# Kernel tuning notes

Measured on AMD Instinct MI355X. Metric: run time of the kernel, lower is better.

The kernel has to match this reference:

```python
import jax, jax.numpy as jnp
import numpy as np


def setup_inputs() -> dict:
    key = jax.random.key(0)
    ks = jax.random.split(key, 6)
    B, T, S, E, D = 8, 128, 512, 512, 512  # batch, trg_len, src_len, enc_dim, trg_dim
    W_SCALE = 0.03  # small init to keep tanh unsaturated
    return {
        "hidden": jax.random.normal(ks[0], (B, T, D), jnp.float32),
        "encoder_outputs": jax.random.normal(ks[1], (B, S, E), jnp.float32),
        "encoder_mask": jnp.ones((B, S), jnp.float32),
        "W_attn": jax.random.normal(ks[2], (D, E + D), jnp.float32) * W_SCALE,
        "b_attn": jnp.zeros((D,), jnp.float32),
        "W_v": jax.random.normal(ks[3], (1, D), jnp.float32) * W_SCALE,
        "b_v": jnp.zeros((1,), jnp.float32),
        "W_out": jax.random.normal(ks[4], (D, E + D), jnp.float32) * W_SCALE,
    }


def masked_softmax(x, m, axis=-1):
    # faithful to repo: x*m, stable exp, e*m, normalize with eps
    x = x * m
    e_x = jnp.exp(x - jnp.max(x, axis=axis, keepdims=True))
    e_x = e_x * m
    return e_x / (jnp.sum(e_x, axis=axis, keepdims=True) + 1e-6)


def reference(hidden, encoder_outputs, encoder_mask, W_attn, b_attn, W_v, b_v, W_out):
    B, T, D = hidden.shape
    S = encoder_outputs.shape[1]
    # concat order in get_energy is (hidden_i, encoder_outputs), so split W_attn
    W_h = W_attn[:, :D]   # (D_out, trg_dim)
    W_e = W_attn[:, D:]   # (D_out, enc_dim)
    # Linear(concat) == h@W_h^T + e@W_e^T + b; vectorized over all (t, s) pairs
    hp = jnp.einsum('btd,kd->btk', hidden, W_h)            # (B,T,K)
    ep = jnp.einsum('bse,ke->bsk', encoder_outputs, W_e)   # (B,S,K)
    feat = jnp.tanh(hp[:, :, None, :] + ep[:, None, :, :] + b_attn)  # (B,T,S,K)
    energies = jnp.einsum('btsk,k->bts', feat, W_v[0]) + b_v[0]      # (B,T,S)
    # forward: energies * mask, then masked softmax
    m = encoder_mask[:, None, :]  # (B,1,S)
    energies = energies * m
    attn_weights = masked_softmax(energies, m, axis=-1)    # (B,T,S)
    weighted_context = jnp.einsum('bts,bse->bte', attn_weights, encoder_outputs)
    h_cat = jnp.concatenate([weighted_context, hidden], axis=-1)  # (B,T,E+D)
    h_tilde = jnp.tanh(jnp.einsum('btc,dc->btd', h_cat, W_out))   # (B,T,D)
    return h_tilde, weighted_context, attn_weights
```

## Files before the change

kernel.cpp:

```cpp
#include <hip/hip_runtime.h>
#include <hip/hip_bf16.h>
#include <math.h>

typedef unsigned short u16;
typedef unsigned int u32;
typedef __bf16 bf16x8 __attribute__((ext_vector_type(8)));
typedef float f32x4 __attribute__((ext_vector_type(4)));

#define OUT_WC   524288LL
#define OUT_ATTN 1048576LL
#define C2 2.8853900817779268f
#define LOG2E 1.4426950408889634f
#define LAS 40

__device__ inline u16 f2b(float f) {
    return (u16)((__float_as_uint(f) + 0x8000u) >> 16);
}
__device__ inline float b2f(u16 v) { return __uint_as_float(((u32)v) << 16); }
__device__ inline u32 pkcvt(float x, float y) {
    __hip_bfloat162 h = __float22bfloat162_rn(make_float2(x, y));
    return *(u32*)&h;
}
__device__ inline float tanh_fast(float x) {
    return 1.f - 2.f * __builtin_amdgcn_rcpf(__builtin_amdgcn_exp2f(C2 * x) + 1.f);
}

__global__ __launch_bounds__(256) void tobf(
    const float* __restrict__ enc, const float* __restrict__ hidden,
    const float* __restrict__ Wattn, const float* __restrict__ Wout,
    u16* __restrict__ dst)
{
    long long i = ((long long)blockIdx.x * 256 + threadIdx.x) * 8;
    const float* src; long long off;
    if (i < 2097152)      { src = enc;    off = i; }
    else if (i < 2621440) { src = hidden; off = i - 2097152; }
    else if (i < 3145728) { src = Wattn;  off = i - 2621440; }
    else                  { src = Wout;   off = i - 3145728; }
    float4 v0 = *(const float4*)(src + off);
    float4 v1 = *(const float4*)(src + off + 4);
    *(uint4*)(dst + i) = make_uint4(pkcvt(v0.x, v0.y), pkcvt(v0.z, v0.w),
                                    pkcvt(v1.x, v1.y), pkcvt(v1.z, v1.w));
}

__global__ __launch_bounds__(256) void proj(
    const u16* __restrict__ hidden_bf, const u16* __restrict__ enc_bf,
    const u16* __restrict__ Wattn_bf, const float* __restrict__ battn,
    const u16* __restrict__ Wout_bf,
    float* __restrict__ hp, u16* __restrict__ ept, float* __restrict__ hh)
{
    __shared__ u16 lA[64 * LAS];
    __shared__ u16 lB[64 * LAS];
    const int tid = threadIdx.x;
    const int wvi = tid >> 6, ln = tid & 63;
    const int wm = wvi >> 1, wn = wvi & 1;
    const int l16 = ln & 15, quad = ln >> 4;
    const int blk = blockIdx.x;
    int bx, by, zz = 0, lda, ldb, mode;
    const u16 *A, *B;
    if (blk < 512) {
        mode = 0;
        zz = blk >> 6; by = (blk >> 3) & 7; bx = blk & 7;
        A = Wattn_bf + 512; lda = 1024;
        B = enc_bf + (long long)zz * 262144; ldb = 512;
    } else if (blk < 640) {
        mode = 1;
        int i = blk - 512; by = i >> 3; bx = i & 7;
        A = hidden_bf; lda = 512;
        B = Wattn_bf; ldb = 1024;
    } else {
        mode = 2;
        int i = blk - 640; by = i >> 3; bx = i & 7;
        A = hidden_bf; lda = 512;
        B = Wout_bf + 512; ldb = 1024;
    }
    const int m0 = by * 64, n0 = bx * 64;
    const int srow = tid >> 2, skof = (tid & 3) * 8;
    const u16* Ap = A + (long long)(m0 + srow) * lda + skof;
    const u16* Bp = B + (long long)(n0 + srow) * ldb + skof;

    f32x4 acc00 = {0,0,0,0}, acc01 = {0,0,0,0}, acc10 = {0,0,0,0}, acc11 = {0,0,0,0};

    for (int k0 = 0; k0 < 512; k0 += 32) {
        uint4 av = *(const uint4*)(Ap + k0);
        uint4 bv = *(const uint4*)(Bp + k0);
        __syncthreads();
        *(uint4*)&lA[srow * LAS + skof] = av;
        *(uint4*)&lB[srow * LAS + skof] = bv;
        __syncthreads();
        bf16x8 a0 = *(const bf16x8*)&lA[(wm * 32      + l16) * LAS + quad * 8];
        bf16x8 a1 = *(const bf16x8*)&lA[(wm * 32 + 16 + l16) * LAS + quad * 8];
        bf16x8 b0 = *(const bf16x8*)&lB[(wn * 32      + l16) * LAS + quad * 8];
        bf16x8 b1 = *(const bf16x8*)&lB[(wn * 32 + 16 + l16) * LAS + quad * 8];
        acc00 = __builtin_amdgcn_mfma_f32_16x16x32_bf16(a0, b0, acc00, 0, 0, 0);
        acc01 = __builtin_amdgcn_mfma_f32_16x16x32_bf16(a0, b1, acc01, 0, 0, 0);
        acc10 = __builtin_amdgcn_mfma_f32_16x16x32_bf16(a1, b0, acc10, 0, 0, 0);
        acc11 = __builtin_amdgcn_mfma_f32_16x16x32_bf16(a1, b1, acc11, 0, 0, 0);
    }

    const f32x4* accs[4] = { &acc00, &acc01, &acc10, &acc11 };
    #pragma unroll
    for (int i = 0; i < 2; ++i) {
        #pragma unroll
        for (int j = 0; j < 2; ++j) {
            const f32x4& a = *accs[i * 2 + j];
            #pragma unroll
            for (int r = 0; r < 4; ++r) {
                int m = m0 + wm * 32 + i * 16 + quad * 4 + r;
                int n = n0 + wn * 32 + j * 16 + l16;
                float v = a[r];
                if (mode == 0)
                    ept[(long long)zz * 262144 + (long long)m * 512 + n] =
                        f2b(__builtin_amdgcn_exp2f(C2 * v));
                else if (mode == 1)
                    hp[(long long)m * 512 + n] = C2 * (v + battn[n]);
                else
                    hh[(long long)m * 512 + n] = v;
            }
        }
    }
}

__device__ inline float wred_sum(float v) {
    #pragma unroll
    for (int i = 32; i > 0; i >>= 1) v += __shfl_xor(v, i);
    return v;
}
__device__ inline float wred_max(float v) {
    #pragma unroll
    for (int i = 32; i > 0; i >>= 1) v = fmaxf(v, __shfl_xor(v, i));
    return v;
}

__device__ inline void proc8(uint4 c, float4 hw, float* a0, float* a1) {
    u32 cc[4] = {c.x, c.y, c.z, c.w};
    #pragma unroll
    for (int i = 0; i < 4; ++i) {
        float xl = __uint_as_float(cc[i] << 16);
        float xh = __uint_as_float(cc[i] & 0xFFFF0000u);
        float rl0 = __builtin_amdgcn_rcpf(fmaf(hw.x, xl, 1.f));
        float rh0 = __builtin_amdgcn_rcpf(fmaf(hw.x, xh, 1.f));
        float rl1 = __builtin_amdgcn_rcpf(fmaf(hw.y, xl, 1.f));
        float rh1 = __builtin_amdgcn_rcpf(fmaf(hw.y, xh, 1.f));
        a0[2*i]   = fmaf(hw.z, rl0, a0[2*i]);
        a0[2*i+1] = fmaf(hw.z, rh0, a0[2*i+1]);
        a1[2*i]   = fmaf(hw.z, rl1, a1[2*i]);
        a1[2*i+1] = fmaf(hw.z, rh1, a1[2*i+1]);
    }
}
__device__ inline void wcproc2(uint4 c, float2 ap, float* acc0, float* acc1) {
    u32 cc[4] = {c.x, c.y, c.z, c.w};
    #pragma unroll
    for (int i = 0; i < 4; ++i) {
        float el = __uint_as_float(cc[i] << 16);
        float eh = __uint_as_float(cc[i] & 0xFFFF0000u);
        acc0[2*i]   = fmaf(ap.x, el, acc0[2*i]);
        acc0[2*i+1] = fmaf(ap.x, eh, acc0[2*i+1]);
        acc1[2*i]   = fmaf(ap.y, el, acc1[2*i]);
        acc1[2*i+1] = fmaf(ap.y, eh, acc1[2*i+1]);
    }
}

__global__ __launch_bounds__(1024) void energies(
    const float* __restrict__ maskp, const float* __restrict__ hp,
    const u16* __restrict__ ept, const float* __restrict__ Wv,
    const float* __restrict__ bvp, const u16* __restrict__ enc_bf,
    float* __restrict__ attn, float* __restrict__ wc)
{
    __shared__ __align__(16) float4 hpw[512];
    __shared__ float pa[2][16][512];
    __shared__ float aL[512][2];
    __shared__ float red[16];
    const int tid = threadIdx.x;
    const int b  = blockIdx.x & 7;
    const int t0 = (blockIdx.x >> 3) * 2;
    const int th = tid >> 9;
    const int k5 = tid & 511;
    const long long row0 = (long long)(b * 128 + t0) * 512;

    float hv = hp[row0 + (long long)th * 512 + k5];
    float eh = __builtin_amdgcn_exp2f(hv);
    float* hpwf = (float*)hpw;
    hpwf[k5 * 4 + th] = eh;
    float w = 0.f;
    if (th == 0) { w = Wv[k5]; hpwf[k5 * 4 + 2] = w; }
    float wsum = wred_sum(w);
    if ((tid & 63) == 0) red[tid >> 6] = wsum;
    __syncthreads();
    float sumWv = 0.f;
    #pragma unroll
    for (int i = 0; i < 16; ++i) sumWv += red[i];

    const int kg = tid >> 6, sl = tid & 63;
    const int s0 = sl * 8;
    const u16* eb = ept + (long long)b * 262144 + (kg * 32) * 512 + s0;
    const float4* hq = &hpw[kg * 32];

    float a0[8] = {0,0,0,0,0,0,0,0}, a1[8] = {0,0,0,0,0,0,0,0};
    uint4 c0 = *(const uint4*)(eb);
    uint4 c1 = *(const uint4*)(eb + 512);
    for (int kk = 0; kk < 30; kk += 2) {
        const u16* nb = eb + (kk + 2) * 512;
        uint4 n0 = *(const uint4*)(nb);
        uint4 n1 = *(const uint4*)(nb + 512);
        proc8(c0, hq[kk],     a0, a1);
        proc8(c1, hq[kk + 1], a0, a1);
        c0 = n0; c1 = n1;
    }
    proc8(c0, hq[30], a0, a1);
    proc8(c1, hq[31], a0, a1);

    *(float4*)&pa[0][kg][s0]     = make_float4(a0[0], a0[1], a0[2], a0[3]);
    *(float4*)&pa[0][kg][s0 + 4] = make_float4(a0[4], a0[5], a0[6], a0[7]);
    *(float4*)&pa[1][kg][s0]     = make_float4(a1[0], a1[1], a1[2], a1[3]);
    *(float4*)&pa[1][kg][s0 + 4] = make_float4(a1[4], a1[5], a1[6], a1[7]);
    __syncthreads();

    float A = 0.f;
    #pragma unroll
    for (int g = 0; g < 16; ++g) A += pa[th][g][k5];
    float mv = maskp[(long long)b * 512 + k5];
    float bv0 = bvp[0];
    float r = (bv0 + sumWv - 2.f * A) * mv; r *= mv;

    float vmax = wred_max(r);
    if ((tid & 63) == 0) red[tid >> 6] = vmax;
    __syncthreads();
    float mx = red[th * 8];
    #pragma unroll
    for (int i = 1; i < 8; ++i) mx = fmaxf(mx, red[th * 8 + i]);

    float ex = __builtin_amdgcn_exp2f((r - mx) * LOG2E) * mv;
    float vsum = wred_sum(ex);
    __syncthreads();
    if ((tid & 63) == 0) red[tid >> 6] = vsum;
    __syncthreads();
    float sm = 0.f;
    #pragma unroll
    for (int i = 0; i < 8; ++i) sm += red[th * 8 + i];
    float at = ex * (1.f / (sm + 1e-6f));
    attn[row0 + (long long)th * 512 + k5] = at;
    aL[k5][th] = at;
    __syncthreads();

    const int eg = tid & 63, sg = tid >> 6;
    const u16* encb = enc_bf + (long long)b * 262144 + (long long)(sg * 32) * 512 + eg * 8;
    const float2* aq = (const float2*)&aL[sg * 32][0];
    float acc0[8] = {0,0,0,0,0,0,0,0}, acc1[8] = {0,0,0,0,0,0,0,0};
    uint4 e0 = *(const uint4*)(encb);
    uint4 e1 = *(const uint4*)(encb + 512);
    for (int j = 0; j < 30; j += 2) {
        uint4 f0 = *(const uint4*)(encb + (long long)(j + 2) * 512);
        uint4 f1 = *(const uint4*)(encb + (long long)(j + 3) * 512);
        wcproc2(e0, aq[j],     acc0, acc1);
        wcproc2(e1, aq[j + 1], acc0, acc1);
        e0 = f0; e1 = f1;
    }
    wcproc2(e0, aq[30], acc0, acc1);
    wcproc2(e1, aq[31], acc0, acc1);

    *(float4*)&pa[0][sg][eg * 8]     = make_float4(acc0[0], acc0[1], acc0[2], acc0[3]);
    *(float4*)&pa[0][sg][eg * 8 + 4] = make_float4(acc0[4], acc0[5], acc0[6], acc0[7]);
    *(float4*)&pa[1][sg][eg * 8]     = make_float4(acc1[0], acc1[1], acc1[2], acc1[3]);
    *(float4*)&pa[1][sg][eg * 8 + 4] = make_float4(acc1[4], acc1[5], acc1[6], acc1[7]);
    __syncthreads();

    float wcv = 0.f;
    #pragma unroll
    for (int g = 0; g < 16; ++g) wcv += pa[th][g][k5];
    wc[row0 + (long long)th * 512 + k5] = wcv;
}

__global__ __launch_bounds__(256) void hout_k(
    const float* __restrict__ wc, const u16* __restrict__ Wout_bf,
    float* __restrict__ out)
{
    __shared__ u16 lA[32 * LAS];
    __shared__ u16 lB[64 * LAS];
    const int tid = threadIdx.x;
    const int wvi = tid >> 6, ln = tid & 63;
    const int l16 = ln & 15, quad = ln >> 4;
    const int msub = wvi & 1, npair = wvi >> 1;
    const int m0 = blockIdx.y * 32, n0 = blockIdx.x * 64;
    const int rowA = tid >> 3, kofA = (tid & 7) * 4;
    const int rowB = tid >> 2, kofB = (tid & 3) * 8;
    f32x4 acc0 = {0,0,0,0}, acc1 = {0,0,0,0};

    for (int k0 = 0; k0 < 512; k0 += 32) {
        float4 av = *(const float4*)(wc + (long long)(m0 + rowA) * 512 + k0 + kofA);
        uint4 bv = *(const uint4*)(Wout_bf + (long long)(n0 + rowB) * 1024 + k0 + kofB);
        __syncthreads();
        *(uint2*)&lA[rowA * LAS + kofA] = make_uint2(pkcvt(av.x, av.y), pkcvt(av.z, av.w));
        int kk = kofB ^ (((rowB >> 3) & 3) << 3);
        *(uint4*)&lB[rowB * LAS + kk] = bv;
        __syncthreads();
        bf16x8 a = *(const bf16x8*)&lA[(msub * 16 + l16) * LAS + quad * 8];
        int nr0 = npair * 32 + l16, nr1 = nr0 + 16;
        bf16x8 b0 = *(const bf16x8*)&lB[nr0 * LAS + (quad * 8 ^ (((nr0 >> 3) & 3) << 3))];
        bf16x8 b1 = *(const bf16x8*)&lB[nr1 * LAS + (quad * 8 ^ (((nr1 >> 3) & 3) << 3))];
        acc0 = __builtin_amdgcn_mfma_f32_16x16x32_bf16(a, b0, acc0, 0, 0, 0);
        acc1 = __builtin_amdgcn_mfma_f32_16x16x32_bf16(a, b1, acc1, 0, 0, 0);
    }
    #pragma unroll
    for (int j = 0; j < 2; ++j) {
        const f32x4& a = j ? acc1 : acc0;
        #pragma unroll
        for (int r = 0; r < 4; ++r) {
            int m = m0 + msub * 16 + quad * 4 + r;
            int n = n0 + npair * 32 + j * 16 + l16;
            long long idx = (long long)m * 512 + n;
            out[idx] = tanh_fast(a[r] + out[idx]);
        }
    }
}

extern "C" void kernel_launch(void* const* d_in, const int* in_sizes, int n_in,
                              void* d_out, int out_size, void* d_ws, size_t ws_size,
                              hipStream_t stream)
{
    const float* hidden = (const float*)d_in[0];
    const float* enc    = (const float*)d_in[1];
    const float* mask   = (const float*)d_in[2];
    const float* Wattn  = (const float*)d_in[3];
    const float* battn  = (const float*)d_in[4];
    const float* Wv     = (const float*)d_in[5];
    const float* bvp    = (const float*)d_in[6];
    const float* Wout   = (const float*)d_in[7];
    float* out = (float*)d_out;

    float* hp  = (float*)d_ws;
    u16*   ept = (u16*)((char*)d_ws + (2 << 20));
    u16*   bfp = (u16*)((char*)d_ws + (6 << 20));
    u16* enc_bf    = bfp;
    u16* hidden_bf = bfp + 2097152;
    u16* Wattn_bf  = bfp + 2621440;
    u16* Wout_bf   = bfp + 3145728;

    tobf<<<1792, 256, 0, stream>>>(enc, hidden, Wattn, Wout, bfp);
    proj<<<768, 256, 0, stream>>>(hidden_bf, enc_bf, Wattn_bf, battn, Wout_bf,
                                  hp, ept, out );
    energies<<<512, 1024, 0, stream>>>(mask, hp, ept, Wv, bvp, enc_bf,
                                       out + OUT_ATTN, out + OUT_WC);
    hout_k<<<dim3(8, 32, 1), 256, 0, stream>>>(out + OUT_WC, Wout_bf, out);
}
```

Before: 146.6 us.

## Fuse bf16 conversion into GEMM loads and use LDS atomics for reductions

Removes the separate fp32-to-bf16 conversion kernel. The projection and output GEMMs now load fp32 directly and convert in registers, and one set of projection blocks writes the bf16 copy of encoder outputs for later use. In the energies kernel, the large 16-way partial-sum LDS buffer is replaced by a small accumulator updated with shared-memory atomicAdd. This cuts LDS footprint, which may raise occupancy, at the cost of atomic contention and doubled global read bytes in the GEMMs.

Measured after the change: 226.5 us. 54.5% more time.

```diff
diff --git a/kernel.cpp b/kernel.cpp
--- a/kernel.cpp
+++ b/kernel.cpp
@@ -25,28 +25,12 @@
     return 1.f - 2.f * __builtin_amdgcn_rcpf(__builtin_amdgcn_exp2f(C2 * x) + 1.f);
 }
 
-__global__ __launch_bounds__(256) void tobf(
-    const float* __restrict__ enc, const float* __restrict__ hidden,
-    const float* __restrict__ Wattn, const float* __restrict__ Wout,
-    u16* __restrict__ dst)
-{
-    long long i = ((long long)blockIdx.x * 256 + threadIdx.x) * 8;
-    const float* src; long long off;
-    if (i < 2097152)      { src = enc;    off = i; }
-    else if (i < 2621440) { src = hidden; off = i - 2097152; }
-    else if (i < 3145728) { src = Wattn;  off = i - 2621440; }
-    else                  { src = Wout;   off = i - 3145728; }
-    float4 v0 = *(const float4*)(src + off);
-    float4 v1 = *(const float4*)(src + off + 4);
-    *(uint4*)(dst + i) = make_uint4(pkcvt(v0.x, v0.y), pkcvt(v0.z, v0.w),
-                                    pkcvt(v1.x, v1.y), pkcvt(v1.z, v1.w));
-}
-
 __global__ __launch_bounds__(256) void proj(
-    const u16* __restrict__ hidden_bf, const u16* __restrict__ enc_bf,
-    const u16* __restrict__ Wattn_bf, const float* __restrict__ battn,
-    const u16* __restrict__ Wout_bf,
-    float* __restrict__ hp, u16* __restrict__ ept, float* __restrict__ hh)
+    const float* __restrict__ hidden, const float* __restrict__ enc,
+    const float* __restrict__ Wattn, const float* __restrict__ battn,
+    const float* __restrict__ Wout,
+    float* __restrict__ hp, u16* __restrict__ ept, float* __restrict__ hh,
+    u16* __restrict__ enc_bf)
 {
     __shared__ u16 lA[64 * LAS];
     __shared__ u16 lB[64 * LAS];
@@ -56,33 +40,43 @@
     const int l16 = ln & 15, quad = ln >> 4;
     const int blk = blockIdx.x;
     int bx, by, zz = 0, lda, ldb, mode;
-    const u16 *A, *B;
+    const float *A, *B;
     if (blk < 512) {
         mode = 0;
         zz = blk >> 6; by = (blk >> 3) & 7; bx = blk & 7;
-        A = Wattn_bf + 512; lda = 1024;
-        B = enc_bf + (long long)zz * 262144; ldb = 512;
+        A = Wattn + 512; lda = 1024;
+        B = enc + (long long)zz * 262144; ldb = 512;
     } else if (blk < 640) {
         mode = 1;
         int i = blk - 512; by = i >> 3; bx = i & 7;
-        A = hidden_bf; lda = 512;
-        B = Wattn_bf; ldb = 1024;
+        A = hidden; lda = 512;
+        B = Wattn; ldb = 1024;
     } else {
         mode = 2;
         int i = blk - 640; by = i >> 3; bx = i & 7;
-        A = hidden_bf; lda = 512;
-        B = Wout_bf + 512; ldb = 1024;
+        A = hidden; lda = 512;
+        B = Wout + 512; ldb = 1024;
     }
     const int m0 = by * 64, n0 = bx * 64;
     const int srow = tid >> 2, skof = (tid & 3) * 8;
-    const u16* Ap = A + (long long)(m0 + srow) * lda + skof;
-    const u16* Bp = B + (long long)(n0 + srow) * ldb + skof;
+    const float* Ap = A + (long long)(m0 + srow) * lda + skof;
+    const float* Bp = B + (long long)(n0 + srow) * ldb + skof;
+    const bool wr_enc = (mode == 0) && (by == 0);
 
     f32x4 acc00 = {0,0,0,0}, acc01 = {0,0,0,0}, acc10 = {0,0,0,0}, acc11 = {0,0,0,0};
 
     for (int k0 = 0; k0 < 512; k0 += 32) {
-        uint4 av = *(const uint4*)(Ap + k0);
-        uint4 bv = *(const uint4*)(Bp + k0);
+        float4 af0 = *(const float4*)(Ap + k0);
+        float4 af1 = *(const float4*)(Ap + k0 + 4);
+        float4 bf0 = *(const float4*)(Bp + k0);
+        float4 bf1 = *(const float4*)(Bp + k0 + 4);
+        uint4 av = make_uint4(pkcvt(af0.x, af0.y), pkcvt(af0.z, af0.w),
+                              pkcvt(af1.x, af1.y), pkcvt(af1.z, af1.w));
+        uint4 bv = make_uint4(pkcvt(bf0.x, bf0.y), pkcvt(bf0.z, bf0.w),
+                              pkcvt(bf1.x, bf1.y), pkcvt(bf1.z, bf1.w));
+        if (wr_enc)
+            *(uint4*)(enc_bf + (long long)zz * 262144 +
+                      (long long)(n0 + srow) * 512 + k0 + skof) = bv;
         __syncthreads();
         *(uint4*)&lA[srow * LAS + skof] = av;
         *(uint4*)&lB[srow * LAS + skof] = bv;
@@ -167,7 +161,7 @@
     float* __restrict__ attn, float* __restrict__ wc)
 {
     __shared__ __align__(16) float4 hpw[512];
-    __shared__ float pa[2][16][512];
+    __shared__ float accE[2][512];
     __shared__ float aL[512][2];
     __shared__ float red[16];
     const int tid = threadIdx.x;
@@ -177,10 +171,11 @@
     const int k5 = tid & 511;
     const long long row0 = (long long)(b * 128 + t0) * 512;
 
+    ((float*)accE)[tid] = 0.f;
     float hv = hp[row0 + (long long)th * 512 + k5];
-    float eh = __builtin_amdgcn_exp2f(hv);
+    float ehv = __builtin_amdgcn_exp2f(hv);
     float* hpwf = (float*)hpw;
-    hpwf[k5 * 4 + th] = eh;
+    hpwf[k5 * 4 + th] = ehv;
     float w = 0.f;
     if (th == 0) { w = Wv[k5]; hpwf[k5 * 4 + 2] = w; }
     float wsum = wred_sum(w);
@@ -209,15 +204,15 @@
     proc8(c0, hq[30], a0, a1);
     proc8(c1, hq[31], a0, a1);
 
-    *(float4*)&pa[0][kg][s0]     = make_float4(a0[0], a0[1], a0[2], a0[3]);
-    *(float4*)&pa[0][kg][s0 + 4] = make_float4(a0[4], a0[5], a0[6], a0[7]);
-    *(float4*)&pa[1][kg][s0]     = make_float4(a1[0], a1[1], a1[2], a1[3]);
-    *(float4*)&pa[1][kg][s0 + 4] = make_float4(a1[4], a1[5], a1[6], a1[7]);
-    __syncthreads();
-
-    float A = 0.f;
-    #pragma unroll
-    for (int g = 0; g < 16; ++g) A += pa[th][g][k5];
+    #pragma unroll
+    for (int i = 0; i < 8; ++i) {
+        int ii = (i + sl) & 7;
+        atomicAdd(&accE[0][s0 + ii], a0[ii]);
+        atomicAdd(&accE[1][s0 + ii], a1[ii]);
+    }
+    __syncthreads();
+
+    float A = accE[th][k5];
     float mv = maskp[(long long)b * 512 + k5];
     float bv0 = bvp[0];
     float r = (bv0 + sumWv - 2.f * A) * mv; r *= mv;
@@ -240,6 +235,7 @@
     float at = ex * (1.f / (sm + 1e-6f));
     attn[row0 + (long long)th * 512 + k5] = at;
     aL[k5][th] = at;
+    ((float*)accE)[tid] = 0.f;
     __syncthreads();
 
     const int eg = tid & 63, sg = tid >> 6;
@@ -258,20 +254,19 @@
     wcproc2(e0, aq[30], acc0, acc1);
     wcproc2(e1, aq[31], acc0, acc1);
 
-    *(float4*)&pa[0][sg][eg * 8]     = make_float4(acc0[0], acc0[1], acc0[2], acc0[3]);
-    *(float4*)&pa[0][sg][eg * 8 + 4] = make_float4(acc0[4], acc0[5], acc0[6], acc0[7]);
-    *(float4*)&pa[1][sg][eg * 8]     = make_float4(acc1[0], acc1[1], acc1[2], acc1[3]);
-    *(float4*)&pa[1][sg][eg * 8 + 4] = make_float4(acc1[4], acc1[5], acc1[6], acc1[7]);
-    __syncthreads();
-
-    float wcv = 0.f;
-    #pragma unroll
-    for (int g = 0; g < 16; ++g) wcv += pa[th][g][k5];
-    wc[row0 + (long long)th * 512 + k5] = wcv;
+    #pragma unroll
+    for (int i = 0; i < 8; ++i) {
+        int ii = (i + eg) & 7;
+        atomicAdd(&accE[0][eg * 8 + ii], acc0[ii]);
+        atomicAdd(&accE[1][eg * 8 + ii], acc1[ii]);
+    }
+    __syncthreads();
+
+    wc[row0 + (long long)th * 512 + k5] = accE[th][k5];
 }
 
 __global__ __launch_bounds__(256) void hout_k(
-    const float* __restrict__ wc, const u16* __restrict__ Wout_bf,
+    const float* __restrict__ wc, const float* __restrict__ Wout,
     float* __restrict__ out)
 {
     __shared__ u16 lA[32 * LAS];
@@ -287,7 +282,10 @@
 
     for (int k0 = 0; k0 < 512; k0 += 32) {
         float4 av = *(const float4*)(wc + (long long)(m0 + rowA) * 512 + k0 + kofA);
-        uint4 bv = *(const uint4*)(Wout_bf + (long long)(n0 + rowB) * 1024 + k0 + kofB);
+        float4 bw0 = *(const float4*)(Wout + (long long)(n0 + rowB) * 1024 + k0 + kofB);
+        float4 bw1 = *(const float4*)(Wout + (long long)(n0 + rowB) * 1024 + k0 + kofB + 4);
+        uint4 bv = make_uint4(pkcvt(bw0.x, bw0.y), pkcvt(bw0.z, bw0.w),
+                              pkcvt(bw1.x, bw1.y), pkcvt(bw1.z, bw1.w));
         __syncthreads();
         *(uint2*)&lA[rowA * LAS + kofA] = make_uint2(pkcvt(av.x, av.y), pkcvt(av.z, av.w));
         int kk = kofB ^ (((rowB >> 3) & 3) << 3);
@@ -327,18 +325,13 @@
     const float* Wout   = (const float*)d_in[7];
     float* out = (float*)d_out;
 
-    float* hp  = (float*)d_ws;
-    u16*   ept = (u16*)((char*)d_ws + (2 << 20));
-    u16*   bfp = (u16*)((char*)d_ws + (6 << 20));
-    u16* enc_bf    = bfp;
-    u16* hidden_bf = bfp + 2097152;
-    u16* Wattn_bf  = bfp + 2621440;
-    u16* Wout_bf   = bfp + 3145728;
-
-    tobf<<<1792, 256, 0, stream>>>(enc, hidden, Wattn, Wout, bfp);
-    proj<<<768, 256, 0, stream>>>(hidden_bf, enc_bf, Wattn_bf, battn, Wout_bf,
-                                  hp, ept, out );
+    float* hp     = (float*)d_ws;
+    u16*   ept    = (u16*)((char*)d_ws + (2 << 20));
+    u16*   enc_bf = (u16*)((char*)d_ws + (6 << 20));
+
+    proj<<<768, 256, 0, stream>>>(hidden, enc, Wattn, battn, Wout,
+                                  hp, ept, out , enc_bf);
     energies<<<512, 1024, 0, stream>>>(mask, hp, ept, Wv, bvp, enc_bf,
                                        out + OUT_ATTN, out + OUT_WC);
-    hout_k<<<dim3(8, 32, 1), 256, 0, stream>>>(out + OUT_WC, Wout_bf, out);
-}
+    hout_k<<<dim3(8, 32, 1), 256, 0, stream>>>(out + OUT_WC, Wout, out);
+}
```
